# Kernel tuning notes

Hardware: AMD Instinct MI355X
Metric: run time of the kernel (lower is better)

## Reference

```python
import jax, jax.numpy as jnp
import numpy as np

N, D, K = 500000, 128, 2048

def setup_inputs() -> dict:
    key = jax.random.key(0)
    kx, kp = jax.random.split(key)
    x = jax.random.normal(kx, (N, D), dtype=jnp.float32)
    p = jax.random.normal(kp, (D,), dtype=jnp.float32)
    return {"x": x, "p": p, "k": K}

def reference(x, p, k):
    # y = x @ p / ||p||  -> [N]
    y = (x @ p) / jnp.linalg.norm(p)
    top_vals, top_idx = jax.lax.top_k(y, k)          # [k], [k]
    # gather top-k rows and scale by tanh of their scores
    out = x[top_idx] * jnp.tanh(top_vals)[:, None]   # [k, D]
    return out
```

## Files before the change

kernel.cpp:

```cpp
#include <hip/hip_runtime.h>


#define HIST_BITS 12
#define HIST_BINS (1 << HIST_BITS)
#define HIST_SHIFT (32 - HIST_BITS)
#define SORTN 8192
#define SLICES 8

__device__ __forceinline__ unsigned mono_key(float f) {
    unsigned u = __float_as_uint(f);
    return (u & 0x80000000u) ? ~u : (u | 0x80000000u);
}
__device__ __forceinline__ float mono_key_inv(unsigned mk) {
    unsigned u = (mk & 0x80000000u) ? (mk ^ 0x80000000u) : ~mk;
    return __uint_as_float(u);
}

__global__ void score_kernel(const float* __restrict__ x, const float* __restrict__ p,
                             float* __restrict__ y, int N, int rpw,
                             unsigned* __restrict__ hz) {
    if (blockIdx.x == 0) {
        for (int i = threadIdx.x; i < HIST_BINS + 1; i += 256) hz[i] = 0u;
    }

    int lane = threadIdx.x & 63;
    int half = lane >> 5;
    int l32  = lane & 31;
    long long gwave = ((long long)blockIdx.x * blockDim.x + threadIdx.x) >> 6;
    long long start = gwave * rpw;
    if (start >= N) return;

    float4 pq = ((const float4*)p)[l32];
    double pp = (double)pq.x * pq.x + (double)pq.y * pq.y +
                (double)pq.z * pq.z + (double)pq.w * pq.w;
    #pragma unroll
    for (int off = 16; off > 0; off >>= 1) pp += __shfl_xor(pp, off, 64);
    double rinv = 1.0 / sqrt(pp);

    long long rend = start + rpw; if (rend > N) rend = N;
    for (long long r0 = start; r0 < rend; r0 += 4) {
        long long rowA = r0 + half;
        long long rowB = r0 + 2 + half;
        bool vb = (r0 + 2) < rend;
        float4 xa = ((const float4*)(x + rowA * 128))[l32];
        float4 xb = vb ? ((const float4*)(x + rowB * 128))[l32]
                       : make_float4(0.f, 0.f, 0.f, 0.f);
        double dA = (double)xa.x * pq.x + (double)xa.y * pq.y +
                    (double)xa.z * pq.z + (double)xa.w * pq.w;
        double dB = (double)xb.x * pq.x + (double)xb.y * pq.y +
                    (double)xb.z * pq.z + (double)xb.w * pq.w;
        #pragma unroll
        for (int off = 16; off > 0; off >>= 1) {
            dA += __shfl_xor(dA, off, 64);
            dB += __shfl_xor(dB, off, 64);
        }
        if (l32 == 0) {
            y[rowA] = (float)(dA * rinv);
            if (vb) y[rowB] = (float)(dB * rinv);
        }
    }
}

__global__ void hist_kernel(const float* __restrict__ y, unsigned* __restrict__ hist, int N) {
    __shared__ unsigned h[4][HIST_BINS];
    for (int i = threadIdx.x; i < 4 * HIST_BINS; i += blockDim.x) h[0][i] = 0;
    __syncthreads();
    int sub = (threadIdx.x >> 6) & 3;
    int stride = gridDim.x * blockDim.x;
    int N4 = N >> 2;
    const float4* y4 = (const float4*)y;
    for (int i = blockIdx.x * blockDim.x + threadIdx.x; i < N4; i += stride) {
        float4 v = y4[i];
        atomicAdd(&h[sub][mono_key(v.x) >> HIST_SHIFT], 1u);
        atomicAdd(&h[sub][mono_key(v.y) >> HIST_SHIFT], 1u);
        atomicAdd(&h[sub][mono_key(v.z) >> HIST_SHIFT], 1u);
        atomicAdd(&h[sub][mono_key(v.w) >> HIST_SHIFT], 1u);
    }
    for (int i = (N & ~3) + blockIdx.x * blockDim.x + threadIdx.x; i < N; i += stride)
        atomicAdd(&h[sub][mono_key(y[i]) >> HIST_SHIFT], 1u);
    __syncthreads();
    for (int i = threadIdx.x; i < HIST_BINS; i += blockDim.x) {
        unsigned v = h[0][i] + h[1][i] + h[2][i] + h[3][i];
        if (v) atomicAdd(&hist[i], v);
    }
}

__global__ void threshold_kernel(const unsigned* __restrict__ hist,
                                 const int* __restrict__ kptr, int* __restrict__ res) {
    __shared__ unsigned wsum[16];
    int t = threadIdx.x;
    int l = t & 63, w = t >> 6;
    uint4 h = ((const uint4*)hist)[t];
    unsigned tot = h.x + h.y + h.z + h.w;
    unsigned v = tot;
    #pragma unroll
    for (int off = 1; off < 64; off <<= 1) {
        unsigned o = __shfl_down(v, off, 64);
        if (l + off < 64) v += o;
    }
    if (l == 0) wsum[w] = v;
    unsigned excl = v - tot;
    __syncthreads();
    unsigned base = 0;
    for (int ww = w + 1; ww < 16; ww++) base += wsum[ww];
    unsigned S4 = base + excl;
    unsigned S3 = S4 + h.w;
    unsigned S2 = S3 + h.z;
    unsigned S1 = S2 + h.y;
    unsigned S0 = S1 + h.x;
    unsigned k = (unsigned)*kptr;
    if (S0 >= k && S1 < k) res[0] = 4 * t;
    if (S1 >= k && S2 < k) res[0] = 4 * t + 1;
    if (S2 >= k && S3 < k) res[0] = 4 * t + 2;
    if (S3 >= k && S4 < k) res[0] = 4 * t + 3;
}

__global__ void compact_kernel(const float* __restrict__ y, const int* __restrict__ res,
                               unsigned long long* __restrict__ pairs, int* __restrict__ cnt,
                               int N) {
    __shared__ int lcnt, lbase;
    if (threadIdx.x == 0) lcnt = 0;
    __syncthreads();
    int B = res[0];
    int N4 = N >> 2;
    int i = blockIdx.x * blockDim.x + threadIdx.x;
    unsigned mk[4];
    int okmask = 0, nloc = 0;
    int base = i * 4;
    if (i < N4) {
        float4 v = ((const float4*)y)[i];
        mk[0] = mono_key(v.x); mk[1] = mono_key(v.y);
        mk[2] = mono_key(v.z); mk[3] = mono_key(v.w);
        #pragma unroll
        for (int j = 0; j < 4; j++)
            if ((int)(mk[j] >> HIST_SHIFT) >= B) { okmask |= 1 << j; nloc++; }
    } else {
        #pragma unroll
        for (int j = 0; j < 4; j++) {
            int idx = base + j;
            if (idx < N) {
                mk[j] = mono_key(y[idx]);
                if ((int)(mk[j] >> HIST_SHIFT) >= B) { okmask |= 1 << j; nloc++; }
            }
        }
    }
    int lpos = 0;
    if (nloc) lpos = atomicAdd(&lcnt, nloc);
    __syncthreads();
    if (threadIdx.x == 0 && lcnt > 0) lbase = atomicAdd(cnt, lcnt);
    __syncthreads();
    if (nloc) {
        int pos = lbase + lpos;
        #pragma unroll
        for (int j = 0; j < 4; j++) {
            if (okmask & (1 << j)) {
                if (pos < SORTN)
                    pairs[pos] = ((unsigned long long)mk[j] << 32) | (unsigned)~(unsigned)(base + j);
                pos++;
            }
        }
    }
}

__global__ void rank_count_kernel(const unsigned long long* __restrict__ pairs,
                                  const int* __restrict__ cnt,
                                  int* __restrict__ rankpart) {
    __shared__ unsigned long long s[SORTN / SLICES];
    int n = *cnt; if (n > SORTN) n = SORTN;
    if ((int)(blockIdx.x * blockDim.x) >= n) return;
    int npad = (n + 4 * SLICES - 1) & ~(4 * SLICES - 1);
    int slen = npad / SLICES;
    int sbeg = blockIdx.y * slen;
    for (int i = threadIdx.x; i < slen; i += blockDim.x) {
        int gi = sbeg + i;
        s[i] = (gi < n) ? pairs[gi] : 0ull;
    }
    __syncthreads();
    int c = blockIdx.x * blockDim.x + threadIdx.x;
    if (c >= n) return;
    unsigned long long my = pairs[c];
    int r = 0;
    for (int i = 0; i < slen; i += 4)
        r += (int)(s[i] > my) + (int)(s[i+1] > my) + (int)(s[i+2] > my) + (int)(s[i+3] > my);
    rankpart[blockIdx.y * SORTN + c] = r;
}

__global__ void rank_scatter_kernel(const unsigned long long* __restrict__ pairs,
                                    const int* __restrict__ cnt,
                                    const int* __restrict__ rankpart,
                                    unsigned long long* __restrict__ spairs, int K) {
    int n = *cnt; if (n > SORTN) n = SORTN;
    int c = blockIdx.x * blockDim.x + threadIdx.x;
    if (c >= n) return;
    int r = 0;
    #pragma unroll
    for (int sl = 0; sl < SLICES; sl++) r += rankpart[sl * SORTN + c];
    if (r < K) spairs[r] = pairs[c];
}

__global__ void gather_kernel(const float* __restrict__ x,
                              const unsigned long long* __restrict__ spairs,
                              float* __restrict__ out, int K) {
    int t = blockIdx.x * blockDim.x + threadIdx.x;
    int j = t >> 5, lane = t & 31;
    if (j >= K) return;
    unsigned long long key = spairs[j];
    float scale = tanhf(mono_key_inv((unsigned)(key >> 32)));
    unsigned idx = ~(unsigned)(key & 0xFFFFFFFFull);
    float4 v = ((const float4*)(x + (size_t)idx * 128))[lane];
    ((float4*)(out + (size_t)j * 128))[lane] =
        make_float4(v.x * scale, v.y * scale, v.z * scale, v.w * scale);
}

extern "C" void kernel_launch(void* const* d_in, const int* in_sizes, int n_in,
                              void* d_out, int out_size, void* d_ws, size_t ws_size,
                              hipStream_t stream) {
    const float* x = (const float*)d_in[0];
    const float* p = (const float*)d_in[1];
    const int*   kptr = (const int*)d_in[2];
    float* out = (float*)d_out;

    const int D = in_sizes[1];
    const int N = in_sizes[0] / D;
    const int K = out_size / D;
    (void)n_in; (void)ws_size;

    unsigned char* w = (unsigned char*)d_ws;
    float* y = (float*)w;
    size_t off = ((size_t)N * sizeof(float) + 255) & ~(size_t)255;
    unsigned* hist = (unsigned*)(w + off);
    int* cnt = (int*)(w + off + HIST_BINS * sizeof(unsigned));
    int* res = cnt + 1;
    size_t off2 = (off + HIST_BINS * sizeof(unsigned) + 3 * sizeof(int) + 255) & ~(size_t)255;
    unsigned long long* pairs = (unsigned long long*)(w + off2);
    unsigned long long* spairs = pairs + SORTN;
    int* rankpart = (int*)(spairs + SORTN);

    {
        const int blocks = 2048;
        long long total_waves = (long long)blocks * 256 / 64;
        int rpw = (int)((N + total_waves - 1) / total_waves);
        rpw = (rpw + 1) & ~1;
        score_kernel<<<blocks, 256, 0, stream>>>(x, p, y, N, rpw, hist);
    }
    hist_kernel<<<64, 1024, 0, stream>>>(y, hist, N);
    threshold_kernel<<<1, 1024, 0, stream>>>(hist, kptr, res);
    {
        int blocks = (((N + 3) / 4) + 255) / 256;
        compact_kernel<<<blocks, 256, 0, stream>>>(y, res, pairs, cnt, N);
    }
    rank_count_kernel<<<dim3(SORTN / 256, SLICES), 256, 0, stream>>>(pairs, cnt, rankpart);
    rank_scatter_kernel<<<SORTN / 256, 256, 0, stream>>>(pairs, cnt, rankpart, spairs, K);
    gather_kernel<<<(K * 32 + 255) / 256, 256, 0, stream>>>(x, spairs, out, K);
}
```

Measured before the change: 377.8 us.

## Fuse threshold into compaction and merge rank, scatter and gather kernels

The threshold search over the histogram now runs redundantly inside every compact block, with each block scanning all 4096 bins itself. The rank-count, rank-scatter and gather kernels become one kernel that holds all candidate pairs in shared memory, sums slice ranks in shared memory and writes the scaled output rows directly. This cuts the pipeline from seven launches to four and removes the rankpart and spairs round trips through global memory. In exchange every compact block reads the whole histogram, and the merged rank kernel uses 64KB+ of shared memory per block.

```diff
diff --git a/kernel.cpp b/kernel.cpp
--- a/kernel.cpp
+++ b/kernel.cpp
@@ -6,6 +6,7 @@
 #define HIST_SHIFT (32 - HIST_BITS)
 #define SORTN 8192
 #define SLICES 8
+#define RBLK 128
 
 __device__ __forceinline__ unsigned mono_key(float f) {
     unsigned u = __float_as_uint(f);
@@ -85,52 +86,60 @@
     }
 }
 
-__global__ void threshold_kernel(const unsigned* __restrict__ hist,
-                                 const int* __restrict__ kptr, int* __restrict__ res) {
-    __shared__ unsigned wsum[16];
-    int t = threadIdx.x;
-    int l = t & 63, w = t >> 6;
-    uint4 h = ((const uint4*)hist)[t];
-    unsigned tot = h.x + h.y + h.z + h.w;
+__global__ void compact_kernel(const float* __restrict__ y, const unsigned* __restrict__ hist,
+                               const int* __restrict__ kptr,
+                               unsigned long long* __restrict__ pairs, int* __restrict__ cnt,
+                               int N) {
+    __shared__ unsigned wsumB[4];
+    __shared__ int sB;
+    __shared__ int lcnt, lbase;
+    if (threadIdx.x == 0) lcnt = 0;
+
+    int N4 = N >> 2;
+    int i = blockIdx.x * blockDim.x + threadIdx.x;
+    int base = i * 4;
+    float4 vy = make_float4(0.f, 0.f, 0.f, 0.f);
+    bool vload = (i < N4);
+    if (vload) vy = ((const float4*)y)[i];
+
+    int t = threadIdx.x, l = t & 63, w = t >> 6;
+    const uint4* H4 = (const uint4*)hist;
+    uint4 a = H4[4 * t + 0], b = H4[4 * t + 1], c4 = H4[4 * t + 2], d4 = H4[4 * t + 3];
+    unsigned hh[16] = {a.x, a.y, a.z, a.w, b.x, b.y, b.z, b.w,
+                       c4.x, c4.y, c4.z, c4.w, d4.x, d4.y, d4.z, d4.w};
+    unsigned tot = 0;
+    #pragma unroll
+    for (int j = 0; j < 16; j++) tot += hh[j];
     unsigned v = tot;
     #pragma unroll
     for (int off = 1; off < 64; off <<= 1) {
         unsigned o = __shfl_down(v, off, 64);
         if (l + off < 64) v += o;
     }
-    if (l == 0) wsum[w] = v;
+    if (l == 0) wsumB[w] = v;
     unsigned excl = v - tot;
     __syncthreads();
-    unsigned base = 0;
-    for (int ww = w + 1; ww < 16; ww++) base += wsum[ww];
-    unsigned S4 = base + excl;
-    unsigned S3 = S4 + h.w;
-    unsigned S2 = S3 + h.z;
-    unsigned S1 = S2 + h.y;
-    unsigned S0 = S1 + h.x;
+    unsigned sbase = 0;
+    #pragma unroll
+    for (int ww = 1; ww < 4; ww++) if (ww > w) sbase += wsumB[ww];
     unsigned k = (unsigned)*kptr;
-    if (S0 >= k && S1 < k) res[0] = 4 * t;
-    if (S1 >= k && S2 < k) res[0] = 4 * t + 1;
-    if (S2 >= k && S3 < k) res[0] = 4 * t + 2;
-    if (S3 >= k && S4 < k) res[0] = 4 * t + 3;
-}
-
-__global__ void compact_kernel(const float* __restrict__ y, const int* __restrict__ res,
-                               unsigned long long* __restrict__ pairs, int* __restrict__ cnt,
-                               int N) {
-    __shared__ int lcnt, lbase;
-    if (threadIdx.x == 0) lcnt = 0;
-    __syncthreads();
-    int B = res[0];
-    int N4 = N >> 2;
-    int i = blockIdx.x * blockDim.x + threadIdx.x;
+    unsigned S = sbase + excl;
+    int Bloc = -1;
+    #pragma unroll
+    for (int j = 15; j >= 0; j--) {
+        unsigned Sj = S + hh[j];
+        if (Sj >= k && S < k) Bloc = 16 * t + j;
+        S = Sj;
+    }
+    if (Bloc >= 0) sB = Bloc;
+    __syncthreads();
+    int B = sB;
+
     unsigned mk[4];
     int okmask = 0, nloc = 0;
-    int base = i * 4;
-    if (i < N4) {
-        float4 v = ((const float4*)y)[i];
-        mk[0] = mono_key(v.x); mk[1] = mono_key(v.y);
-        mk[2] = mono_key(v.z); mk[3] = mono_key(v.w);
+    if (vload) {
+        mk[0] = mono_key(vy.x); mk[1] = mono_key(vy.y);
+        mk[2] = mono_key(vy.z); mk[3] = mono_key(vy.w);
         #pragma unroll
         for (int j = 0; j < 4; j++)
             if ((int)(mk[j] >> HIST_SHIFT) >= B) { okmask |= 1 << j; nloc++; }
@@ -162,54 +171,59 @@
     }
 }
 
-__global__ void rank_count_kernel(const unsigned long long* __restrict__ pairs,
-                                  const int* __restrict__ cnt,
-                                  int* __restrict__ rankpart) {
-    __shared__ unsigned long long s[SORTN / SLICES];
+__global__ void rank_kernel(const unsigned long long* __restrict__ pairs,
+                            const int* __restrict__ cnt,
+                            const float* __restrict__ x,
+                            float* __restrict__ out, int K) {
+    __shared__ unsigned long long s[SORTN];
+    __shared__ int rp[SLICES][RBLK];
+    __shared__ int s_rr[RBLK];
+    __shared__ unsigned s_idx[RBLK];
+    __shared__ float s_sc[RBLK];
+
     int n = *cnt; if (n > SORTN) n = SORTN;
-    if ((int)(blockIdx.x * blockDim.x) >= n) return;
-    int npad = (n + 4 * SLICES - 1) & ~(4 * SLICES - 1);
+    if ((int)(blockIdx.x * RBLK) >= n) return;
+    int npad = (n + 31) & ~31;
+
+    for (int i = threadIdx.x; i < npad; i += 1024)
+        s[i] = (i < n) ? pairs[i] : 0ull;
+    __syncthreads();
+
+    int cl = threadIdx.x & (RBLK - 1);
+    int sl = threadIdx.x >> 7;
+    int c  = blockIdx.x * RBLK + cl;
+    unsigned long long my = (c < n) ? s[c] : 0ull;
     int slen = npad / SLICES;
-    int sbeg = blockIdx.y * slen;
-    for (int i = threadIdx.x; i < slen; i += blockDim.x) {
-        int gi = sbeg + i;
-        s[i] = (gi < n) ? pairs[gi] : 0ull;
-    }
-    __syncthreads();
-    int c = blockIdx.x * blockDim.x + threadIdx.x;
-    if (c >= n) return;
-    unsigned long long my = pairs[c];
+    int sbeg = sl * slen;
     int r = 0;
-    for (int i = 0; i < slen; i += 4)
+    for (int i = sbeg; i < sbeg + slen; i += 4)
         r += (int)(s[i] > my) + (int)(s[i+1] > my) + (int)(s[i+2] > my) + (int)(s[i+3] > my);
-    rankpart[blockIdx.y * SORTN + c] = r;
-}
-
-__global__ void rank_scatter_kernel(const unsigned long long* __restrict__ pairs,
-                                    const int* __restrict__ cnt,
-                                    const int* __restrict__ rankpart,
-                                    unsigned long long* __restrict__ spairs, int K) {
-    int n = *cnt; if (n > SORTN) n = SORTN;
-    int c = blockIdx.x * blockDim.x + threadIdx.x;
-    if (c >= n) return;
-    int r = 0;
-    #pragma unroll
-    for (int sl = 0; sl < SLICES; sl++) r += rankpart[sl * SORTN + c];
-    if (r < K) spairs[r] = pairs[c];
-}
-
-__global__ void gather_kernel(const float* __restrict__ x,
-                              const unsigned long long* __restrict__ spairs,
-                              float* __restrict__ out, int K) {
-    int t = blockIdx.x * blockDim.x + threadIdx.x;
-    int j = t >> 5, lane = t & 31;
-    if (j >= K) return;
-    unsigned long long key = spairs[j];
-    float scale = tanhf(mono_key_inv((unsigned)(key >> 32)));
-    unsigned idx = ~(unsigned)(key & 0xFFFFFFFFull);
-    float4 v = ((const float4*)(x + (size_t)idx * 128))[lane];
-    ((float4*)(out + (size_t)j * 128))[lane] =
-        make_float4(v.x * scale, v.y * scale, v.z * scale, v.w * scale);
+    rp[sl][cl] = r;
+    __syncthreads();
+
+    if (sl == 0) {
+        int rr = 0;
+        #pragma unroll
+        for (int q = 0; q < SLICES; q++) rr += rp[q][cl];
+        bool sel = (c < n) && (rr < K);
+        s_rr[cl] = sel ? rr : -1;
+        if (sel) {
+            unsigned mk  = (unsigned)(my >> 32);
+            s_idx[cl] = ~(unsigned)(my & 0xFFFFFFFFull);
+            s_sc[cl]  = tanhf(mono_key_inv(mk));
+        }
+    }
+    __syncthreads();
+
+    for (int q = threadIdx.x; q < RBLK * 32; q += 1024) {
+        int c2 = q >> 5, lane = q & 31;
+        int rr = s_rr[c2];
+        if (rr < 0) continue;
+        float sc = s_sc[c2];
+        float4 v = ((const float4*)(x + (size_t)s_idx[c2] * 128))[lane];
+        ((float4*)(out + (size_t)rr * 128))[lane] =
+            make_float4(v.x * sc, v.y * sc, v.z * sc, v.w * sc);
+    }
 }
 
 extern "C" void kernel_launch(void* const* d_in, const int* in_sizes, int n_in,
@@ -230,11 +244,8 @@
     size_t off = ((size_t)N * sizeof(float) + 255) & ~(size_t)255;
     unsigned* hist = (unsigned*)(w + off);
     int* cnt = (int*)(w + off + HIST_BINS * sizeof(unsigned));
-    int* res = cnt + 1;
-    size_t off2 = (off + HIST_BINS * sizeof(unsigned) + 3 * sizeof(int) + 255) & ~(size_t)255;
+    size_t off2 = (off + (HIST_BINS + 1) * sizeof(unsigned) + 255) & ~(size_t)255;
     unsigned long long* pairs = (unsigned long long*)(w + off2);
-    unsigned long long* spairs = pairs + SORTN;
-    int* rankpart = (int*)(spairs + SORTN);
 
     {
         const int blocks = 2048;
@@ -244,12 +255,9 @@
         score_kernel<<<blocks, 256, 0, stream>>>(x, p, y, N, rpw, hist);
     }
     hist_kernel<<<64, 1024, 0, stream>>>(y, hist, N);
-    threshold_kernel<<<1, 1024, 0, stream>>>(hist, kptr, res);
     {
         int blocks = (((N + 3) / 4) + 255) / 256;
-        compact_kernel<<<blocks, 256, 0, stream>>>(y, res, pairs, cnt, N);
-    }
-    rank_count_kernel<<<dim3(SORTN / 256, SLICES), 256, 0, stream>>>(pairs, cnt, rankpart);
-    rank_scatter_kernel<<<SORTN / 256, 256, 0, stream>>>(pairs, cnt, rankpart, spairs, K);
-    gather_kernel<<<(K * 32 + 255) / 256, 256, 0, stream>>>(x, spairs, out, K);
-}
+        compact_kernel<<<blocks, 256, 0, stream>>>(y, hist, kptr, pairs, cnt, N);
+    }
+    rank_kernel<<<SORTN / RBLK, 1024, 0, stream>>>(pairs, cnt, x, out, K);
+}
```

Measured after the change: 377.2 us. Within noise of the previous version (-0.2%).
